# Performance work log

Measured on AMD Instinct MI355X. Metric: run time of the kernel, lower is better.

The kernel has to match this reference:

```python
import jax, jax.numpy as jnp
import numpy as np

N_CHANNELS = 29
HIDDEN = [5, 4, 4]
IN_FEAT = 7
OUT_FEAT = 3
EPS = 1e-07


def _glorot(key, fan_in, fan_out, shape):
    lim = np.sqrt(6.0 / (fan_in + fan_out))
    return jax.random.uniform(key, shape, jnp.float32, -lim, lim)


def _make_params(key):
    # Batched per-channel weights: stack n_channels tiny MLPs along leading dim.
    sizes = [IN_FEAT] + HIDDEN + [OUT_FEAT]
    Ws, bs = [], []
    for i in range(len(sizes) - 1):
        key, k = jax.random.split(key)
        Ws.append(_glorot(k, sizes[i], sizes[i + 1], (N_CHANNELS, sizes[i], sizes[i + 1])))
        bs.append(jnp.zeros((N_CHANNELS, sizes[i + 1]), jnp.float32))
    return Ws, bs


def setup_inputs() -> dict:
    key = jax.random.key(0)
    ks = jax.random.split(key, 16)
    N = 262144
    inp = {
        "tau": jax.random.uniform(ks[0], (N, N_CHANNELS, 1), jnp.float32),
        "mu": jax.random.uniform(ks[1], (N, 1), jnp.float32, 0.05, 1.0),
        "mu_bar": jax.random.uniform(ks[2], (N, 1), jnp.float32, 0.05, 1.0),
        "lw": jax.random.uniform(ks[3], (N, 1), jnp.float32),
        "h2o": jax.random.uniform(ks[4], (N, 1), jnp.float32),
        "o3": jax.random.uniform(ks[5], (N, 1), jnp.float32),
        "co2": jax.random.uniform(ks[6], (N, 1), jnp.float32),
        "u": jax.random.uniform(ks[7], (N, 1), jnp.float32),
        "n2o": jax.random.uniform(ks[8], (N, 1), jnp.float32),
        "ch4": jax.random.uniform(ks[9], (N, 1), jnp.float32),
    }
    Wd, bd = _make_params(ks[10])
    Wf, bf = _make_params(ks[11])
    for i in range(4):
        inp[f"Wd{i}"] = Wd[i]
        inp[f"bd{i}"] = bd[i]
        inp[f"Wf{i}"] = Wf[i]
        inp[f"bf{i}"] = bf[i]
    return inp


def _mlp(x, Ws, bs):
    # x: [N, F]; Ws[i]: [C, fin, fout]; output [N, C, 3]
    h = jnp.einsum('nf,cfh->nch', x, Ws[0]) + bs[0]
    h = jax.nn.relu(h)
    for i in (1, 2):
        h = jnp.einsum('nch,chk->nck', h, Ws[i]) + bs[i]
        h = jax.nn.relu(h)
    h = jnp.einsum('nch,chk->nck', h, Ws[3]) + bs[3]
    return jax.nn.softmax(h, axis=-1)


def reference(tau, mu, mu_bar, lw, h2o, o3, co2, u, n2o, ch4,
              Wd0, bd0, Wd1, bd1, Wd2, bd2, Wd3, bd3,
              Wf0, bf0, Wf1, bf1, Wf2, bf2, Wf3, bf3):
    constituents = jnp.concatenate([lw, h2o, o3, co2, u, n2o, ch4], axis=1)  # [N,7]
    c_direct = constituents / (mu + EPS)
    c_diffuse = constituents / (mu_bar + EPS)
    mu3 = mu[:, :, None]          # [N,1,1]
    mu_bar3 = mu_bar[:, :, None]
    tau_total = jnp.sum(tau, axis=-1, keepdims=True)  # [N,C,1]
    t_direct = jnp.exp(-tau_total / (mu3 + EPS))       # [N,C,1]
    t_diffuse = jnp.exp(-tau_total / (mu_bar3 + EPS))
    e_direct = _mlp(c_direct, [Wd0, Wd1, Wd2, Wd3], [bd0, bd1, bd2, bd3])    # [N,C,3]
    e_diffuse = _mlp(c_diffuse, [Wf0, Wf1, Wf2, Wf3], [bf0, bf1, bf2, bf3])  # [N,C,3]
    return jnp.concatenate([t_direct, t_diffuse, e_direct, e_diffuse], axis=2)  # [N,C,8]
```

## Files before the change

kernel.cpp:

```cpp
#include <hip/hip_runtime.h>

#define EPS 1e-7f
#define NCH 29
#define SPB 128
#define ROWA 17


typedef float f32x2 __attribute__((ext_vector_type(2)));

__device__ __forceinline__ f32x2 splat2(float v) { f32x2 r; r.x = v; r.y = v; return r; }
__device__ __forceinline__ f32x2 fma2(f32x2 a, f32x2 b, f32x2 c) {
    return __builtin_elementwise_fma(a, b, c);
}
__device__ __forceinline__ f32x2 max2(f32x2 a, f32x2 b) {
    return __builtin_elementwise_max(a, b);
}
__device__ __forceinline__ f32x2 expc2(f32x2 a) {
    f32x2 r; r.x = __expf(a.x); r.y = __expf(a.y); return r;
}
__device__ __forceinline__ f32x2 rcp2(f32x2 a) {
    f32x2 r; r.x = __builtin_amdgcn_rcpf(a.x); r.y = __builtin_amdgcn_rcpf(a.y); return r;
}

__device__ __forceinline__ void barrier_lds_only() {
    asm volatile("s_waitcnt lgkmcnt(0)\n\ts_barrier" ::: "memory");
}

__device__ __forceinline__ void mlp7p(const f32x2 x[7],
    const float* __restrict__ W0, const float* __restrict__ b0,
    const float* __restrict__ W1, const float* __restrict__ b1,
    const float* __restrict__ W2, const float* __restrict__ b2,
    const float* __restrict__ W3, const float* __restrict__ b3,
    f32x2 e[3])
{
    const f32x2 zero = splat2(0.0f);
    f32x2 h0[5];
#pragma unroll
    for (int h = 0; h < 5; ++h) {
        f32x2 a = splat2(b0[h]);
#pragma unroll
        for (int f = 0; f < 7; ++f) a = fma2(x[f], splat2(W0[f * 5 + h]), a);
        h0[h] = max2(a, zero);
    }
    f32x2 h1[4];
#pragma unroll
    for (int k = 0; k < 4; ++k) {
        f32x2 a = splat2(b1[k]);
#pragma unroll
        for (int h = 0; h < 5; ++h) a = fma2(h0[h], splat2(W1[h * 4 + k]), a);
        h1[k] = max2(a, zero);
    }
    f32x2 h2[4];
#pragma unroll
    for (int k = 0; k < 4; ++k) {
        f32x2 a = splat2(b2[k]);
#pragma unroll
        for (int h = 0; h < 4; ++h) a = fma2(h1[h], splat2(W2[h * 4 + k]), a);
        h2[k] = max2(a, zero);
    }
    f32x2 l[3];
#pragma unroll
    for (int k = 0; k < 3; ++k) {
        f32x2 a = splat2(b3[k]);
#pragma unroll
        for (int h = 0; h < 4; ++h) a = fma2(h2[h], splat2(W3[h * 3 + k]), a);
        l[k] = a;
    }
    f32x2 m = max2(l[0], max2(l[1], l[2]));
    f32x2 e0 = expc2(l[0] - m);
    f32x2 e1 = expc2(l[1] - m);
    f32x2 e2 = expc2(l[2] - m);
    f32x2 rs = rcp2(e0 + e1 + e2);
    e[0] = e0 * rs; e[1] = e1 * rs; e[2] = e2 * rs;
}

__global__ __launch_bounds__(512, 6) void lps_kernel(
    const float* __restrict__ tau, const float* __restrict__ mu, const float* __restrict__ mu_bar,
    const float* __restrict__ lw, const float* __restrict__ h2o, const float* __restrict__ o3,
    const float* __restrict__ co2, const float* __restrict__ uu, const float* __restrict__ n2o,
    const float* __restrict__ ch4,
    const float* __restrict__ Wd0, const float* __restrict__ bd0,
    const float* __restrict__ Wf0, const float* __restrict__ bf0,
    const float* __restrict__ Wd1, const float* __restrict__ bd1,
    const float* __restrict__ Wf1, const float* __restrict__ bf1,
    const float* __restrict__ Wd2, const float* __restrict__ bd2,
    const float* __restrict__ Wf2, const float* __restrict__ bf2,
    const float* __restrict__ Wd3, const float* __restrict__ bd3,
    const float* __restrict__ Wf3, const float* __restrict__ bf3,
    float* __restrict__ out, int N)
{
    __shared__ __align__(16) float4 obuf[SPB * ROWA];

    const int tid  = threadIdx.x;
    const int lane = tid & 63;
    const int wid  = __builtin_amdgcn_readfirstlane(tid >> 6);

    const long long base = (long long)blockIdx.x * SPB;
    const int s0 = (int)base + lane;
    const int s1 = s0 + 64;
    const int i0 = (s0 < N) ? s0 : (N - 1);
    const int i1 = (s1 < N) ? s1 : (N - 1);

    f32x2 mu2, mub2;
    mu2.x  = mu[i0];      mu2.y  = mu[i1];
    mub2.x = mu_bar[i0];  mub2.y = mu_bar[i1];
    const f32x2 rmu2  = rcp2(mu2 + splat2(EPS));
    const f32x2 rmub2 = rcp2(mub2 + splat2(EPS));

    f32x2 cons2[7];
    cons2[0].x = lw[i0];  cons2[0].y = lw[i1];
    cons2[1].x = h2o[i0]; cons2[1].y = h2o[i1];
    cons2[2].x = o3[i0];  cons2[2].y = o3[i1];
    cons2[3].x = co2[i0]; cons2[3].y = co2[i1];
    cons2[4].x = uu[i0];  cons2[4].y = uu[i1];
    cons2[5].x = n2o[i0]; cons2[5].y = n2o[i1];
    cons2[6].x = ch4[i0]; cons2[6].y = ch4[i1];

    int nsamp = N - (int)base;
    if (nsamp > SPB) nsamp = SPB;
    float4* out4 = (float4*)out;

#pragma unroll
    for (int k = 0; k < 4; ++k) {
        const int c = k * 8 + wid;
        if (c < NCH) {
            f32x2 tau2;
            tau2.x = tau[(size_t)i0 * NCH + c];
            tau2.y = tau[(size_t)i1 * NCH + c];
            const f32x2 td2 = expc2(-(tau2 * rmu2));
            const f32x2 tf2 = expc2(-(tau2 * rmub2));

            f32x2 x2[7];
            f32x2 ed[3], ef[3];
#pragma unroll
            for (int f = 0; f < 7; ++f) x2[f] = cons2[f] * rmu2;
            mlp7p(x2, Wd0 + c * 35, bd0 + c * 5, Wd1 + c * 20, bd1 + c * 4,
                      Wd2 + c * 16, bd2 + c * 4, Wd3 + c * 12, bd3 + c * 3, ed);
#pragma unroll
            for (int f = 0; f < 7; ++f) x2[f] = cons2[f] * rmub2;
            mlp7p(x2, Wf0 + c * 35, bf0 + c * 5, Wf1 + c * 20, bf1 + c * 4,
                      Wf2 + c * 16, bf2 + c * 4, Wf3 + c * 12, bf3 + c * 3, ef);

            const int r = (c - k * 8) * 2;
            obuf[lane * ROWA + r]            = make_float4(td2.x, tf2.x, ed[0].x, ed[1].x);
            obuf[lane * ROWA + r + 1]        = make_float4(ed[2].x, ef[0].x, ef[1].x, ef[2].x);
            obuf[(lane + 64) * ROWA + r]     = make_float4(td2.y, tf2.y, ed[0].y, ed[1].y);
            obuf[(lane + 64) * ROWA + r + 1] = make_float4(ed[2].y, ef[0].y, ef[1].y, ef[2].y);
        }

        barrier_lds_only();

        if (nsamp > 0) {
            if (k < 3) {
                const int tot = nsamp * 16;
                for (int i = tid; i < tot; i += 512) {
                    const int s = i >> 4, rr = i & 15;
                    out4[(base + s) * 58 + k * 16 + rr] = obuf[s * ROWA + rr];
                }
            } else {
                const int tot = nsamp * 10;
                for (int i = tid; i < tot; i += 512) {
                    const int s = i / 10, rr = i - s * 10;
                    out4[(base + s) * 58 + 48 + rr] = obuf[s * ROWA + rr];
                }
            }
        }

        barrier_lds_only();
    }
}

extern "C" void kernel_launch(void* const* d_in, const int* in_sizes, int n_in,
                              void* d_out, int out_size, void* d_ws, size_t ws_size,
                              hipStream_t stream) {
    const float* tau    = (const float*)d_in[0];
    const float* mu     = (const float*)d_in[1];
    const float* mu_bar = (const float*)d_in[2];
    const float* lw     = (const float*)d_in[3];
    const float* h2o    = (const float*)d_in[4];
    const float* o3     = (const float*)d_in[5];
    const float* co2    = (const float*)d_in[6];
    const float* uu     = (const float*)d_in[7];
    const float* n2o    = (const float*)d_in[8];
    const float* ch4    = (const float*)d_in[9];

    const float* Wd0 = (const float*)d_in[10];
    const float* bd0 = (const float*)d_in[11];
    const float* Wf0 = (const float*)d_in[12];
    const float* bf0 = (const float*)d_in[13];
    const float* Wd1 = (const float*)d_in[14];
    const float* bd1 = (const float*)d_in[15];
    const float* Wf1 = (const float*)d_in[16];
    const float* bf1 = (const float*)d_in[17];
    const float* Wd2 = (const float*)d_in[18];
    const float* bd2 = (const float*)d_in[19];
    const float* Wf2 = (const float*)d_in[20];
    const float* bf2 = (const float*)d_in[21];
    const float* Wd3 = (const float*)d_in[22];
    const float* bd3 = (const float*)d_in[23];
    const float* Wf3 = (const float*)d_in[24];
    const float* bf3 = (const float*)d_in[25];

    float* out = (float*)d_out;
    int N = in_sizes[1];

    int blocks = (N + SPB - 1) / SPB;
    lps_kernel<<<blocks, 512, 0, stream>>>(
        tau, mu, mu_bar, lw, h2o, o3, co2, uu, n2o, ch4,
        Wd0, bd0, Wf0, bf0, Wd1, bd1, Wf1, bf1,
        Wd2, bd2, Wf2, bf2, Wd3, bd3, Wf3, bf3,
        out, N);
}
```

Before: 80.21 us.

## Run per-channel MLPs in packed fp16 with pre-packed half-precision weights

```diff
diff --git a/kernel.cpp b/kernel.cpp
--- a/kernel.cpp
+++ b/kernel.cpp
@@ -6,72 +6,114 @@
 #define ROWA 17
 
 
-typedef float f32x2 __attribute__((ext_vector_type(2)));
+typedef float    f32x2 __attribute__((ext_vector_type(2)));
+typedef _Float16 f16;
+typedef f16      f16x2 __attribute__((ext_vector_type(2)));
 
 __device__ __forceinline__ f32x2 splat2(float v) { f32x2 r; r.x = v; r.y = v; return r; }
-__device__ __forceinline__ f32x2 fma2(f32x2 a, f32x2 b, f32x2 c) {
-    return __builtin_elementwise_fma(a, b, c);
-}
-__device__ __forceinline__ f32x2 max2(f32x2 a, f32x2 b) {
-    return __builtin_elementwise_max(a, b);
-}
 __device__ __forceinline__ f32x2 expc2(f32x2 a) {
     f32x2 r; r.x = __expf(a.x); r.y = __expf(a.y); return r;
 }
 __device__ __forceinline__ f32x2 rcp2(f32x2 a) {
     f32x2 r; r.x = __builtin_amdgcn_rcpf(a.x); r.y = __builtin_amdgcn_rcpf(a.y); return r;
 }
+__device__ __forceinline__ f16x2 hbc(unsigned w) { return __builtin_bit_cast(f16x2, w); }
+__device__ __forceinline__ f16x2 hfma(f16x2 a, f16x2 b, f16x2 c) {
+    return __builtin_elementwise_fma(a, b, c);
+}
+__device__ __forceinline__ f16x2 hmax(f16x2 a, f16x2 b) {
+    return __builtin_elementwise_max(a, b);
+}
 
 __device__ __forceinline__ void barrier_lds_only() {
     asm volatile("s_waitcnt lgkmcnt(0)\n\ts_barrier" ::: "memory");
 }
 
-__device__ __forceinline__ void mlp7p(const f32x2 x[7],
-    const float* __restrict__ W0, const float* __restrict__ b0,
-    const float* __restrict__ W1, const float* __restrict__ b1,
-    const float* __restrict__ W2, const float* __restrict__ b2,
-    const float* __restrict__ W3, const float* __restrict__ b3,
-    f32x2 e[3])
+__global__ void wprep_kernel(
+    const float* __restrict__ Wd0, const float* __restrict__ bd0,
+    const float* __restrict__ Wd1, const float* __restrict__ bd1,
+    const float* __restrict__ Wd2, const float* __restrict__ bd2,
+    const float* __restrict__ Wd3, const float* __restrict__ bd3,
+    const float* __restrict__ Wf0, const float* __restrict__ bf0,
+    const float* __restrict__ Wf1, const float* __restrict__ bf1,
+    const float* __restrict__ Wf2, const float* __restrict__ bf2,
+    const float* __restrict__ Wf3, const float* __restrict__ bf3,
+    unsigned* __restrict__ ws)
 {
-    const f32x2 zero = splat2(0.0f);
-    f32x2 h0[5];
+    const int i = blockIdx.x * blockDim.x + threadIdx.x;
+    const int TOT = 2 * NCH * 99;
+    if (i >= TOT) return;
+    const int set = i / (NCH * 99);
+    const int r   = i - set * (NCH * 99);
+    const int c   = r / 99;
+    const int o   = r - c * 99;
+
+    const float* W0 = set ? Wf0 : Wd0; const float* B0 = set ? bf0 : bd0;
+    const float* W1 = set ? Wf1 : Wd1; const float* B1 = set ? bf1 : bd1;
+    const float* W2 = set ? Wf2 : Wd2; const float* B2 = set ? bf2 : bd2;
+    const float* W3 = set ? Wf3 : Wd3; const float* B3 = set ? bf3 : bd3;
+
+    float v;
+    if      (o < 35) v = W0[c * 35 + o];
+    else if (o < 40) v = B0[c * 5  + (o - 35)];
+    else if (o < 60) v = W1[c * 20 + (o - 40)];
+    else if (o < 64) v = B1[c * 4  + (o - 60)];
+    else if (o < 80) v = W2[c * 16 + (o - 64)];
+    else if (o < 84) v = B2[c * 4  + (o - 80)];
+    else if (o < 96) v = W3[c * 12 + (o - 84)];
+    else             v = B3[c * 3  + (o - 96)];
+
+    const unsigned short h = __builtin_bit_cast(unsigned short, (f16)v);
+    ws[i] = (unsigned)h | ((unsigned)h << 16);
+}
+
+__device__ __forceinline__ void mlp7h(const f16x2 x[7],
+    const unsigned* __restrict__ wb, f32x2 e[3])
+{
+    f16x2 zero; zero.x = (f16)0; zero.y = (f16)0;
+    f16x2 h0[5];
 #pragma unroll
     for (int h = 0; h < 5; ++h) {
-        f32x2 a = splat2(b0[h]);
-#pragma unroll
-        for (int f = 0; f < 7; ++f) a = fma2(x[f], splat2(W0[f * 5 + h]), a);
-        h0[h] = max2(a, zero);
-    }
-    f32x2 h1[4];
+        f16x2 a = hbc(wb[35 + h]);
+#pragma unroll
+        for (int f = 0; f < 7; ++f) a = hfma(x[f], hbc(wb[f * 5 + h]), a);
+        h0[h] = hmax(a, zero);
+    }
+    f16x2 h1[4];
 #pragma unroll
     for (int k = 0; k < 4; ++k) {
-        f32x2 a = splat2(b1[k]);
-#pragma unroll
-        for (int h = 0; h < 5; ++h) a = fma2(h0[h], splat2(W1[h * 4 + k]), a);
-        h1[k] = max2(a, zero);
-    }
-    f32x2 h2[4];
+        f16x2 a = hbc(wb[60 + k]);
+#pragma unroll
+        for (int f = 0; f < 5; ++f) a = hfma(h0[f], hbc(wb[40 + f * 4 + k]), a);
+        h1[k] = hmax(a, zero);
+    }
+    f16x2 h2[4];
 #pragma unroll
     for (int k = 0; k < 4; ++k) {
-        f32x2 a = splat2(b2[k]);
-#pragma unroll
-        for (int h = 0; h < 4; ++h) a = fma2(h1[h], splat2(W2[h * 4 + k]), a);
-        h2[k] = max2(a, zero);
-    }
-    f32x2 l[3];
+        f16x2 a = hbc(wb[80 + k]);
+#pragma unroll
+        for (int f = 0; f < 4; ++f) a = hfma(h1[f], hbc(wb[64 + f * 4 + k]), a);
+        h2[k] = hmax(a, zero);
+    }
+    f16x2 l[3];
 #pragma unroll
     for (int k = 0; k < 3; ++k) {
-        f32x2 a = splat2(b3[k]);
-#pragma unroll
-        for (int h = 0; h < 4; ++h) a = fma2(h2[h], splat2(W3[h * 3 + k]), a);
+        f16x2 a = hbc(wb[96 + k]);
+#pragma unroll
+        for (int f = 0; f < 4; ++f) a = hfma(h2[f], hbc(wb[84 + f * 3 + k]), a);
         l[k] = a;
     }
-    f32x2 m = max2(l[0], max2(l[1], l[2]));
-    f32x2 e0 = expc2(l[0] - m);
-    f32x2 e1 = expc2(l[1] - m);
-    f32x2 e2 = expc2(l[2] - m);
-    f32x2 rs = rcp2(e0 + e1 + e2);
-    e[0] = e0 * rs; e[1] = e1 * rs; e[2] = e2 * rs;
+    const float l0x = (float)l[0].x, l1x = (float)l[1].x, l2x = (float)l[2].x;
+    const float l0y = (float)l[0].y, l1y = (float)l[1].y, l2y = (float)l[2].y;
+    const float mx = fmaxf(l0x, fmaxf(l1x, l2x));
+    const float my = fmaxf(l0y, fmaxf(l1y, l2y));
+    const float e0x = __expf(l0x - mx), e1x = __expf(l1x - mx), e2x = __expf(l2x - mx);
+    const float e0y = __expf(l0y - my), e1y = __expf(l1y - my), e2y = __expf(l2y - my);
+    const float rsx = __builtin_amdgcn_rcpf(e0x + e1x + e2x);
+    const float rsy = __builtin_amdgcn_rcpf(e0y + e1y + e2y);
+    e[0].x = e0x * rsx; e[0].y = e0y * rsy;
+    e[1].x = e1x * rsx; e[1].y = e1y * rsy;
+    e[2].x = e2x * rsx; e[2].y = e2y * rsy;
 }
 
 __global__ __launch_bounds__(512, 6) void lps_kernel(
@@ -79,14 +121,7 @@
     const float* __restrict__ lw, const float* __restrict__ h2o, const float* __restrict__ o3,
     const float* __restrict__ co2, const float* __restrict__ uu, const float* __restrict__ n2o,
     const float* __restrict__ ch4,
-    const float* __restrict__ Wd0, const float* __restrict__ bd0,
-    const float* __restrict__ Wf0, const float* __restrict__ bf0,
-    const float* __restrict__ Wd1, const float* __restrict__ bd1,
-    const float* __restrict__ Wf1, const float* __restrict__ bf1,
-    const float* __restrict__ Wd2, const float* __restrict__ bd2,
-    const float* __restrict__ Wf2, const float* __restrict__ bf2,
-    const float* __restrict__ Wd3, const float* __restrict__ bd3,
-    const float* __restrict__ Wf3, const float* __restrict__ bf3,
+    const unsigned* __restrict__ wh,
     float* __restrict__ out, int N)
 {
     __shared__ __align__(16) float4 obuf[SPB * ROWA];
@@ -107,14 +142,16 @@
     const f32x2 rmu2  = rcp2(mu2 + splat2(EPS));
     const f32x2 rmub2 = rcp2(mub2 + splat2(EPS));
 
-    f32x2 cons2[7];
-    cons2[0].x = lw[i0];  cons2[0].y = lw[i1];
-    cons2[1].x = h2o[i0]; cons2[1].y = h2o[i1];
-    cons2[2].x = o3[i0];  cons2[2].y = o3[i1];
-    cons2[3].x = co2[i0]; cons2[3].y = co2[i1];
-    cons2[4].x = uu[i0];  cons2[4].y = uu[i1];
-    cons2[5].x = n2o[i0]; cons2[5].y = n2o[i1];
-    cons2[6].x = ch4[i0]; cons2[6].y = ch4[i1];
+    f16x2 xdh[7], xfh[7];
+    {
+        float c0, c1;
+#define MKX(idx, arr) \
+        c0 = arr[i0]; c1 = arr[i1]; \
+        xdh[idx].x = (f16)(c0 * rmu2.x);  xdh[idx].y = (f16)(c1 * rmu2.y); \
+        xfh[idx].x = (f16)(c0 * rmub2.x); xfh[idx].y = (f16)(c1 * rmub2.y);
+        MKX(0, lw) MKX(1, h2o) MKX(2, o3) MKX(3, co2) MKX(4, uu) MKX(5, n2o) MKX(6, ch4)
+#undef MKX
+    }
 
     int nsamp = N - (int)base;
     if (nsamp > SPB) nsamp = SPB;
@@ -130,16 +167,9 @@
             const f32x2 td2 = expc2(-(tau2 * rmu2));
             const f32x2 tf2 = expc2(-(tau2 * rmub2));
 
-            f32x2 x2[7];
             f32x2 ed[3], ef[3];
-#pragma unroll
-            for (int f = 0; f < 7; ++f) x2[f] = cons2[f] * rmu2;
-            mlp7p(x2, Wd0 + c * 35, bd0 + c * 5, Wd1 + c * 20, bd1 + c * 4,
-                      Wd2 + c * 16, bd2 + c * 4, Wd3 + c * 12, bd3 + c * 3, ed);
-#pragma unroll
-            for (int f = 0; f < 7; ++f) x2[f] = cons2[f] * rmub2;
-            mlp7p(x2, Wf0 + c * 35, bf0 + c * 5, Wf1 + c * 20, bf1 + c * 4,
-                      Wf2 + c * 16, bf2 + c * 4, Wf3 + c * 12, bf3 + c * 3, ef);
+            mlp7h(xdh, wh + c * 99, ed);
+            mlp7h(xfh, wh + (NCH + c) * 99, ef);
 
             const int r = (c - k * 8) * 2;
             obuf[lane * ROWA + r]            = make_float4(td2.x, tf2.x, ed[0].x, ed[1].x);
@@ -202,12 +232,16 @@
     const float* bf3 = (const float*)d_in[25];
 
     float* out = (float*)d_out;
+    unsigned* wh = (unsigned*)d_ws;
     int N = in_sizes[1];
+
+    const int TOT = 2 * NCH * 99;
+    wprep_kernel<<<(TOT + 255) / 256, 256, 0, stream>>>(
+        Wd0, bd0, Wd1, bd1, Wd2, bd2, Wd3, bd3,
+        Wf0, bf0, Wf1, bf1, Wf2, bf2, Wf3, bf3, wh);
 
     int blocks = (N + SPB - 1) / SPB;
     lps_kernel<<<blocks, 512, 0, stream>>>(
         tau, mu, mu_bar, lw, h2o, o3, co2, uu, n2o, ch4,
-        Wd0, bd0, Wf0, bf0, Wd1, bd1, Wf1, bf1,
-        Wd2, bd2, Wf2, bf2, Wd3, bd3, Wf3, bf3,
-        out, N);
-}
+        wh, out, N);
+}
```

After: 82.74 us. 1.03x slower.
